# Kernel optimization log

Hardware: AMD Instinct MI355X
Metric: run time of the kernel (lower is better)

The kernel has to match this reference:

```python
import jax, jax.numpy as jnp
import numpy as np

B, S, E, H = 2, 2048, 1024, 16
DK = E // H


def setup_inputs() -> dict:
    key = jax.random.key(0)
    ks = jax.random.split(key, 10)
    x = jax.random.normal(ks[0], (B, S, E), dtype=jnp.float32)
    mask = jax.random.randint(ks[1], (B, S, S), 0, 2).astype(bool)
    scale = 1.0 / np.sqrt(E)
    def lin(k):
        kw, kb = jax.random.split(k)
        W = jax.random.uniform(kw, (E, E), minval=-scale, maxval=scale, dtype=jnp.float32)
        b = jax.random.uniform(kb, (E,), minval=-scale, maxval=scale, dtype=jnp.float32)
        return W, b
    Wq, bq = lin(ks[2])
    Wk, bk = lin(ks[3])
    Wv, bv = lin(ks[4])
    Wo, bo = lin(ks[5])
    return {"x": x, "mask": mask, "Wq": Wq, "bq": bq, "Wk": Wk, "bk": bk,
            "Wv": Wv, "bv": bv, "Wo": Wo, "bo": bo}


def reference(x, mask, Wq, bq, Wk, bk, Wv, bv, Wo, bo):
    # projections (torch Linear: y = x @ W.T + b)
    q = x @ Wq.T + bq
    k = x @ Wk.T + bk
    v = x @ Wv.T + bv
    # separate heads: [B,S,E] -> [B,H,S,DK]
    def split(t):
        return t.reshape(B, S, H, DK).transpose(0, 2, 1, 3)
    q, k, v = split(q), split(k), split(v)
    scores = jnp.einsum("bhqd,bhkd->bhqk", q, k) / jnp.sqrt(jnp.float32(DK))
    # masked_fill: positions where mask is True get -1e9 (mask broadcast over heads)
    scores = jnp.where(mask[:, None, :, :], jnp.float32(-1e9), scores)
    attn = jax.nn.softmax(scores, axis=-1)  # dropout is identity in eval
    out = jnp.einsum("bhqk,bhkd->bhqd", attn, v)
    out = out.transpose(0, 2, 1, 3).reshape(B, S, E)  # combine heads
    return out @ Wo.T + bo
```

## Files before the change

kernel.cpp:

```cpp
#include <hip/hip_runtime.h>
#include <hip/hip_bf16.h>


typedef __attribute__((ext_vector_type(8))) short short8;
typedef __attribute__((ext_vector_type(4))) short s16x4;
typedef __attribute__((ext_vector_type(4))) float f32x4;
typedef __attribute__((ext_vector_type(2))) unsigned uint32x2;

#define MFMA16(a, b, c) __builtin_amdgcn_mfma_f32_16x16x32_bf16(a, b, c, 0, 0, 0)

#define BATCH 2
#define SEQ   2048
#define EMB   1024
#define HEADS 16
#define DKK   64
#define MROWS (BATCH * SEQ)

typedef __hip_bfloat16 bf16;
typedef unsigned long long u64;

static __device__ __forceinline__ short bf16b(float f) {
    union { bf16 h; short s; } u;
    u.h = __float2bfloat16(f);
    return u.s;
}
static __device__ __forceinline__ unsigned cvtpk(float lo, float hi) {
    unsigned r;
    asm("v_cvt_pk_bf16_f32 %0, %1, %2" : "=v"(r) : "v"(lo), "v"(hi));
    return r;
}
static __device__ __forceinline__ short8 ld8k(const bf16* p) {
    return *(const short8*)p;
}
static __device__ __forceinline__ short8 ld8kf(const float* p) {
    const f32x4 a = *(const f32x4*)p;
    const f32x4 b = *(const f32x4*)(p + 4);
    short8 r;
    r[0] = bf16b(a[0]); r[1] = bf16b(a[1]); r[2] = bf16b(a[2]); r[3] = bf16b(a[3]);
    r[4] = bf16b(b[0]); r[5] = bf16b(b[1]); r[6] = bf16b(b[2]); r[7] = bf16b(b[3]);
    return r;
}

static __device__ __forceinline__ void glds16(const bf16* g, bf16* l) {
    __builtin_amdgcn_global_load_lds(
        (const __attribute__((address_space(1))) void*)g,
        (__attribute__((address_space(3))) void*)l, 16, 0, 0);
}

__global__ void detect_kernel(const unsigned int* __restrict__ mw,
                              int* __restrict__ flags) {
    __shared__ int mbyte;
    if (threadIdx.x == 0) mbyte = 0;
    __syncthreads();
    int mb = 0;
    for (int i = threadIdx.x; i < 4096; i += 256)
        if (mw[i] > 1u) mb = 1;
    if (mb) atomicOr(&mbyte, 1);
    __syncthreads();
    if (threadIdx.x == 0) { flags[0] = 1; flags[1] = mbyte; }
}

__global__ __launch_bounds__(256) void pack_mask(
        const void* __restrict__ mp, unsigned* __restrict__ Mp,
        const int* __restrict__ flags) {
    const bool m8 = flags[1] != 0;
    const int T = blockIdx.x * 256 + threadIdx.x;
    const int lane = T & 63, rest = T >> 6;
    const int wvv = rest & 7;
    const int qb  = (rest >> 3) & 15;
    const int it  = (rest >> 7) & 31;
    const int b   = rest >> 12;
    const int l16 = lane & 15, quad = lane >> 4;
    const int q = qb * 128 + wvv * 16 + l16;
    const size_t rowb = ((size_t)(b * 2048 + q)) * 2048;
    const int k0 = it * 64 + quad * 4;

    unsigned out[4];
    if (m8) {
        const unsigned char* p8 = (const unsigned char*)mp;
#pragma unroll
        for (int j = 0; j < 4; ++j) {
            const unsigned v = *(const unsigned*)(p8 + rowb + k0 + j * 16);
            unsigned w = 0;
#pragma unroll
            for (int r = 0; r < 4; ++r)
                w |= ((((v >> (8 * r)) & 0xFFu) == 0u) ? 0xFFu : 0u) << (8 * r);
            out[j] = w;
        }
    } else {
        const int* p32 = (const int*)mp;
#pragma unroll
        for (int j = 0; j < 4; ++j) {
            const int4 v = *(const int4*)(p32 + rowb + k0 + j * 16);
            unsigned w = 0;
            w |=  (v.x == 0) ? 0xFFu : 0u;
            w |= ((v.y == 0) ? 0xFFu : 0u) << 8;
            w |= ((v.z == 0) ? 0xFFu : 0u) << 16;
            w |= ((v.w == 0) ? 0xFFu : 0u) << 24;
            out[j] = w;
        }
    }
    uint4* dst = (uint4*)(Mp + (size_t)rest * 256 + lane * 4);
    *dst = make_uint4(out[0], out[1], out[2], out[3]);
}

__global__ __launch_bounds__(256) void cvt_all(
        const float* __restrict__ x,  const float* __restrict__ wq,
        const float* __restrict__ wk, const float* __restrict__ wv,
        const float* __restrict__ wo,
        bf16* __restrict__ xb,  bf16* __restrict__ wqb,
        bf16* __restrict__ wkb, bf16* __restrict__ wvb,
        bf16* __restrict__ wob) {
    const int bid = blockIdx.x;
    const float* s; bf16* d; int base;
    if (bid < 2048)      { s = x;  d = xb;  base = bid; }
    else if (bid < 2560) { s = wq; d = wqb; base = bid - 2048; }
    else if (bid < 3072) { s = wk; d = wkb; base = bid - 2560; }
    else if (bid < 3584) { s = wv; d = wvb; base = bid - 3072; }
    else                 { s = wo; d = wob; base = bid - 3584; }
    const int i = (base * 256 + threadIdx.x) * 8;
    *(short8*)(d + i) = ld8kf(s + i);
}

__global__ __launch_bounds__(256) void gemm_qkv_staged(
        const bf16* __restrict__ X,
        const bf16* __restrict__ Wq, const bf16* __restrict__ Wk,
        const bf16* __restrict__ Wv,
        const float* __restrict__ bq, const float* __restrict__ bk,
        const float* __restrict__ bv,
        bf16* __restrict__ qo, bf16* __restrict__ ko, bf16* __restrict__ vo) {
    __shared__ bf16 As[2][128 * 32];
    __shared__ bf16 Bs[2][128 * 32];

    const int t = threadIdx.x, lane = t & 63;
    const int wv = t >> 6;
    const int mb = blockIdx.x / 24, nb = blockIdx.x % 24;
    const int m0 = mb * 128;
    const int n0g = nb * 128;
    const int sel = n0g >> 10;
    const int n0 = n0g & 1023;
    const bf16* W     = sel == 0 ? Wq : (sel == 1 ? Wk : Wv);
    const float* bias = sel == 0 ? bq : (sel == 1 ? bk : bv);
    bf16* out         = sel == 0 ? qo : (sel == 1 ? ko : vo);
    const float oscale = sel == 0 ? 0.18033688011f : 1.0f;

    const int wr = wv >> 1, wc = wv & 1;
    const int m_off = wr * 64, n_off = wc * 64;
    const int l16 = lane & 15, quad = lane >> 4;

    int srow[2], sg[2];
#pragma unroll
    for (int i = 0; i < 2; ++i) {
        const int c = i * 256 + t;
        srow[i] = c >> 2;
        sg[i]   = (c & 3) ^ (srow[i] & 3);
    }

    f32x4 acc[4][4];
#pragma unroll
    for (int i = 0; i < 4; ++i)
#pragma unroll
        for (int j = 0; j < 4; ++j)
            acc[i][j] = (f32x4){0.f, 0.f, 0.f, 0.f};

#pragma unroll
    for (int i = 0; i < 2; ++i) {
        glds16(X + (m0 + srow[i]) * 1024 + sg[i] * 8, &As[0][(i * 256 + t) * 8]);
        glds16(W + (n0 + srow[i]) * 1024 + sg[i] * 8, &Bs[0][(i * 256 + t) * 8]);
    }

    for (int it = 0; it < 32; ++it) {
        __syncthreads();
        if (it < 31) {
            const int ktn = (it + 1) * 32;
            const int nb_ = (it + 1) & 1;
#pragma unroll
            for (int i = 0; i < 2; ++i) {
                glds16(X + (m0 + srow[i]) * 1024 + ktn + sg[i] * 8,
                       &As[nb_][(i * 256 + t) * 8]);
                glds16(W + (n0 + srow[i]) * 1024 + ktn + sg[i] * 8,
                       &Bs[nb_][(i * 256 + t) * 8]);
            }
        }
        const bf16* Ab = As[it & 1];
        const bf16* Bb = Bs[it & 1];
        short8 af[4], bfr[4];
#pragma unroll
        for (int ii = 0; ii < 4; ++ii) {
            const int row = m_off + ii * 16 + l16;
            const int slot = quad ^ (row & 3);
            af[ii] = *(const short8*)(Ab + row * 32 + slot * 8);
        }
#pragma unroll
        for (int jj = 0; jj < 4; ++jj) {
            const int row = n_off + jj * 16 + l16;
            const int slot = quad ^ (row & 3);
            bfr[jj] = *(const short8*)(Bb + row * 32 + slot * 8);
        }
#pragma unroll
        for (int ii = 0; ii < 4; ++ii)
#pragma unroll
            for (int jj = 0; jj < 4; ++jj)
                acc[ii][jj] = MFMA16(af[ii], bfr[jj], acc[ii][jj]);
    }

#pragma unroll
    for (int j = 0; j < 4; ++j) {
        const int nl = n0 + n_off + j * 16 + l16;
        const float bj = bias[nl];
        const int h = nl >> 6, d = nl & 63;
#pragma unroll
        for (int i = 0; i < 4; ++i) {
#pragma unroll
            for (int r = 0; r < 4; ++r) {
                const int m = m0 + m_off + i * 16 + quad * 4 + r;
                const float v = (acc[i][j][r] + bj) * oscale;
                const int bb = m >> 11, ss = m & 2047;
                const int idx = (sel == 2)
                    ? ((bb * HEADS + h) * DKK + d) * SEQ + ss
                    : ((bb * HEADS + h) * SEQ + ss) * DKK + d;
                out[idx] = __float2bfloat16(v);
            }
        }
    }
}

__global__ __launch_bounds__(256) void gemm_out_staged(
        const bf16* __restrict__ X,
        const bf16* __restrict__ W, const float* __restrict__ bias,
        float* __restrict__ out) {
    __shared__ bf16 As[2][128 * 32];
    __shared__ bf16 Bs[2][64 * 32];

    const int t = threadIdx.x, lane = t & 63;
    const int wv = t >> 6;
    const int mb = blockIdx.x >> 4, nb = blockIdx.x & 15;
    const int m0 = mb * 128, n0 = nb * 64;
    const int wr = wv >> 1, wc = wv & 1;
    const int m_off = wr * 64, n_off = wc * 32;
    const int l16 = lane & 15, quad = lane >> 4;

    int srow[2], sg[2];
#pragma unroll
    for (int i = 0; i < 2; ++i) {
        const int c = i * 256 + t;
        srow[i] = c >> 2;
        sg[i]   = (c & 3) ^ (srow[i] & 3);
    }
    const int brow = t >> 2;
    const int bslot = (t & 3) ^ (brow & 3);

    f32x4 acc[4][2];
#pragma unroll
    for (int i = 0; i < 4; ++i)
#pragma unroll
        for (int j = 0; j < 2; ++j)
            acc[i][j] = (f32x4){0.f, 0.f, 0.f, 0.f};

#pragma unroll
    for (int i = 0; i < 2; ++i)
        glds16(X + (m0 + srow[i]) * 1024 + sg[i] * 8, &As[0][(i * 256 + t) * 8]);
    glds16(W + (n0 + brow) * 1024 + bslot * 8, &Bs[0][t * 8]);

    for (int it = 0; it < 32; ++it) {
        __syncthreads();
        if (it < 31) {
            const int ktn = (it + 1) * 32;
            const int nb_ = (it + 1) & 1;
#pragma unroll
            for (int i = 0; i < 2; ++i)
                glds16(X + (m0 + srow[i]) * 1024 + ktn + sg[i] * 8,
                       &As[nb_][(i * 256 + t) * 8]);
            glds16(W + (n0 + brow) * 1024 + ktn + bslot * 8, &Bs[nb_][t * 8]);
        }
        const bf16* Ab = As[it & 1];
        const bf16* Bb = Bs[it & 1];
        short8 af[4], bfr[2];
#pragma unroll
        for (int ii = 0; ii < 4; ++ii) {
            const int row = m_off + ii * 16 + l16;
            const int slot = quad ^ (row & 3);
            af[ii] = *(const short8*)(Ab + row * 32 + slot * 8);
        }
#pragma unroll
        for (int jj = 0; jj < 2; ++jj) {
            const int row = n_off + jj * 16 + l16;
            const int slot = quad ^ (row & 3);
            bfr[jj] = *(const short8*)(Bb + row * 32 + slot * 8);
        }
#pragma unroll
        for (int ii = 0; ii < 4; ++ii)
#pragma unroll
            for (int jj = 0; jj < 2; ++jj)
                acc[ii][jj] = MFMA16(af[ii], bfr[jj], acc[ii][jj]);
    }

#pragma unroll
    for (int j = 0; j < 2; ++j) {
        const int n = n0 + n_off + j * 16 + l16;
        const float bj = bias[n];
#pragma unroll
        for (int i = 0; i < 4; ++i) {
#pragma unroll
            for (int r = 0; r < 4; ++r) {
                const int m = m0 + m_off + i * 16 + quad * 4 + r;
                out[m * 1024 + n] = acc[i][j][r] + bj;
            }
        }
    }
}

__global__ __launch_bounds__(512, 4) void attn_kernel(
        const bf16* __restrict__ Qw,
        const bf16* __restrict__ Kw,
        const bf16* __restrict__ Vw,
        const unsigned* __restrict__ Mp,
        bf16* __restrict__ attn_out) {
    const int t = threadIdx.x;
    const int lane = t & 63;
    const int wv   = t >> 6;
    const int l16 = lane & 15, quad = lane >> 4;
    const int h = blockIdx.y, b = blockIdx.z;
    const int bh = b * HEADS + h;
    const int qb = blockIdx.x;
    const int qb0 = qb * 128;

    const bf16* Q  = Qw + bh * SEQ * DKK;
    const bf16* Kp = Kw + bh * SEQ * DKK;
    const bf16* Vt = Vw + bh * DKK * SEQ;

    __shared__ bf16 Ks[2][4096];
    __shared__ bf16 Vs[2][4096];
    __shared__ bf16 lds_p[8][16][72];

    short8 qf[2];
#pragma unroll
    for (int t2 = 0; t2 < 2; ++t2)
        qf[t2] = ld8k(Q + (qb0 + wv * 16 + l16) * DKK + t2 * 32 + quad * 8);

    const short ob = bf16b(1.0f);
    short8 ones;
#pragma unroll
    for (int e = 0; e < 8; ++e) ones[e] = ob;

    f32x4 o[4];
#pragma unroll
    for (int jd = 0; jd < 4; ++jd) o[jd] = (f32x4){0.f, 0.f, 0.f, 0.f};
    f32x4 lacc = (f32x4){0.f, 0.f, 0.f, 0.f};
    const f32x4 zacc = (f32x4){0.f, 0.f, 0.f, 0.f};

    const int srow = t >> 3;
    const int sg   = (t & 7) ^ (srow & 7);

    glds16(Kp + srow * DKK + sg * 8, &Ks[0][t * 8]);
    glds16(Vt + srow * SEQ + sg * 8, &Vs[0][t * 8]);

    const unsigned* mp_it = Mp + ((size_t)(b * 512 + qb) * 2048 + wv * 256 + lane * 4);

    for (int it = 0; it < SEQ / 64; ++it) {
        __syncthreads();
        if (it < SEQ / 64 - 1) {
            const int nb_ = (it + 1) & 1;
            const int ktn = (it + 1) * 64;
            glds16(Kp + (ktn + srow) * DKK + sg * 8, &Ks[nb_][t * 8]);
            glds16(Vt + srow * SEQ + ktn + sg * 8, &Vs[nb_][t * 8]);
        }

        const uint4 m4 = *(const uint4*)mp_it;
        mp_it += 32768;
        const unsigned m32[4] = {m4.x, m4.y, m4.z, m4.w};

        const bf16* Kb = Ks[it & 1];
        const bf16* Vb = Vs[it & 1];

        short8 kf[2][4];
#pragma unroll
        for (int t2 = 0; t2 < 2; ++t2)
#pragma unroll
            for (int j = 0; j < 4; ++j) {
                const int row = j * 16 + l16;
                const int slot = (t2 * 4 + quad) ^ (row & 7);
                kf[t2][j] = *(const short8*)(Kb + row * 64 + slot * 8);
            }

        f32x4 s[4];
        __builtin_amdgcn_s_setprio(1);
#pragma unroll
        for (int j = 0; j < 4; ++j) {
            s[j] = MFMA16(kf[0][j], qf[0], zacc);
            s[j] = MFMA16(kf[1][j], qf[1], s[j]);
        }
        __builtin_amdgcn_s_setprio(0);

#pragma unroll
        for (int j = 0; j < 4; ++j) {
            const float p0 = __builtin_exp2f(s[j][0]);
            const float p1 = __builtin_exp2f(s[j][1]);
            const float p2 = __builtin_exp2f(s[j][2]);
            const float p3 = __builtin_exp2f(s[j][3]);
            uint32x2 pw;
            pw[0] = cvtpk(p0, p1) & __builtin_amdgcn_perm(0u, m32[j], 0x01010000u);
            pw[1] = cvtpk(p2, p3) & __builtin_amdgcn_perm(0u, m32[j], 0x03030202u);
            *(uint32x2*)(&lds_p[wv][l16][j * 16 + quad * 4]) = pw;
        }

        __builtin_amdgcn_s_setprio(1);
#pragma unroll
        for (int t2 = 0; t2 < 2; ++t2) {
            short8 vf[4];
#pragma unroll
            for (int jd = 0; jd < 4; ++jd) {
                const int row = jd * 16 + l16;
                const int slot = (t2 * 4 + quad) ^ (row & 7);
                vf[jd] = *(const short8*)(Vb + row * 64 + slot * 8);
            }
            const short8 pf = *(const short8*)(&lds_p[wv][l16][t2 * 32 + quad * 8]);
            lacc = MFMA16(pf, ones, lacc);
#pragma unroll
            for (int jd = 0; jd < 4; ++jd)
                o[jd] = MFMA16(pf, vf[jd], o[jd]);
        }
        __builtin_amdgcn_s_setprio(0);
    }

#pragma unroll
    for (int r = 0; r < 4; ++r) {
        const float inv = 1.0f / lacc[r];
        const int q = qb0 + wv * 16 + quad * 4 + r;
#pragma unroll
        for (int jd = 0; jd < 4; ++jd)
            attn_out[(b * SEQ + q) * EMB + h * DKK + jd * 16 + l16] =
                __float2bfloat16(o[jd][r] * inv);
    }
}

extern "C" void kernel_launch(void* const* d_in, const int* in_sizes, int n_in,
                              void* d_out, int out_size, void* d_ws, size_t ws_size,
                              hipStream_t stream) {
    char* ws = (char*)d_ws;
    const size_t MB = 1024 * 1024;
    int*      flags = (int*)ws;
    bf16*     wob   = (bf16*)(ws + 256);
    bf16*     wqb   = (bf16*)(ws + 256 + 2 * MB);
    bf16*     wkb   = (bf16*)(ws + 256 + 4 * MB);
    bf16*     wvb   = (bf16*)(ws + 256 + 6 * MB);
    unsigned* Mp    = (unsigned*)(ws + 256 + 2 * MB);
    bf16*     xb    = (bf16*)(ws + 256 + 10 * MB);
    bf16*     k_ws  = (bf16*)(ws + 256 + 18 * MB);
    bf16*     attn_ws = xb;

    bf16* q_ws = (bf16*)d_out;
    bf16* v_ws = (bf16*)d_out + 4194304;

    detect_kernel<<<1, 256, 0, stream>>>((const unsigned int*)d_in[1], flags);

    cvt_all<<<4096, 256, 0, stream>>>(
        (const float*)d_in[0], (const float*)d_in[2], (const float*)d_in[4],
        (const float*)d_in[6], (const float*)d_in[8],
        xb, wqb, wkb, wvb, wob);

    gemm_qkv_staged<<<768, 256, 0, stream>>>(
        xb, wqb, wkb, wvb,
        (const float*)d_in[3], (const float*)d_in[5], (const float*)d_in[7],
        q_ws, k_ws, v_ws);

    pack_mask<<<2048, 256, 0, stream>>>(d_in[1], Mp, flags);

    attn_kernel<<<dim3(SEQ / 128, HEADS, BATCH), 512, 0, stream>>>(
        q_ws, k_ws, v_ws, Mp, attn_ws);

    gemm_out_staged<<<512, 256, 0, stream>>>(
        attn_ws, wob, (const float*)d_in[9], (float*)d_out);
}
```

Measured before the change: 249.9 us.

## Switch attention to 32x32x16 MFMA with register-resident P via permlane32 swap

Rewrites the attention kernel so each wave handles 32 query rows using 32x32x16 bf16 MFMAs instead of 16x16x32. The P tile is kept in registers and rearranged into the B-operand layout with v_permlane32_swap, removing the per-wave LDS round-trip for probabilities. The block shrinks to 4 waves with each thread staging two K/V chunks, and the mask packing kernel is relaid out to match the new fragment layout. Occupancy hints and register pressure change, since the 16-element accumulators raise VGPR use.

```diff
diff --git a/kernel.cpp b/kernel.cpp
--- a/kernel.cpp
+++ b/kernel.cpp
@@ -3,21 +3,19 @@
 
 
 typedef __attribute__((ext_vector_type(8))) short short8;
-typedef __attribute__((ext_vector_type(4))) short s16x4;
 typedef __attribute__((ext_vector_type(4))) float f32x4;
-typedef __attribute__((ext_vector_type(2))) unsigned uint32x2;
+typedef __attribute__((ext_vector_type(16))) float f32x16;
 
 #define MFMA16(a, b, c) __builtin_amdgcn_mfma_f32_16x16x32_bf16(a, b, c, 0, 0, 0)
+#define MFMA32(a, b, c) __builtin_amdgcn_mfma_f32_32x32x16_bf16(a, b, c, 0, 0, 0)
 
 #define BATCH 2
 #define SEQ   2048
 #define EMB   1024
 #define HEADS 16
 #define DKK   64
-#define MROWS (BATCH * SEQ)
 
 typedef __hip_bfloat16 bf16;
-typedef unsigned long long u64;
 
 static __device__ __forceinline__ short bf16b(float f) {
     union { bf16 h; short s; } u;
@@ -28,6 +26,9 @@
     unsigned r;
     asm("v_cvt_pk_bf16_f32 %0, %1, %2" : "=v"(r) : "v"(lo), "v"(hi));
     return r;
+}
+static __device__ __forceinline__ void swap32(unsigned &a, unsigned &b) {
+    asm("v_permlane32_swap_b32 %0, %1" : "+v"(a), "+v"(b));
 }
 static __device__ __forceinline__ short8 ld8k(const bf16* p) {
     return *(const short8*)p;
@@ -65,43 +66,47 @@
         const int* __restrict__ flags) {
     const bool m8 = flags[1] != 0;
     const int T = blockIdx.x * 256 + threadIdx.x;
-    const int lane = T & 63, rest = T >> 6;
-    const int wvv = rest & 7;
-    const int qb  = (rest >> 3) & 15;
-    const int it  = (rest >> 7) & 31;
-    const int b   = rest >> 12;
-    const int l16 = lane & 15, quad = lane >> 4;
-    const int q = qb * 128 + wvv * 16 + l16;
+    const int lane = T & 63, g = T >> 6;
+    const int wvv = g & 3;
+    const int qb  = (g >> 2) & 15;
+    const int it  = (g >> 6) & 31;
+    const int b   = g >> 11;
+    const int l32 = lane & 31, hi = lane >> 5;
+    const int q = qb * 128 + wvv * 32 + l32;
     const size_t rowb = ((size_t)(b * 2048 + q)) * 2048;
-    const int k0 = it * 64 + quad * 4;
-
-    unsigned out[4];
+
+    unsigned out[8];
     if (m8) {
         const unsigned char* p8 = (const unsigned char*)mp;
 #pragma unroll
-        for (int j = 0; j < 4; ++j) {
-            const unsigned v = *(const unsigned*)(p8 + rowb + k0 + j * 16);
+        for (int k = 0; k < 8; ++k) {
+            const int kb = k >> 2, tt = (k >> 1) & 1, u = k & 1;
+            const int key0 = it * 64 + kb * 32 + tt * 16 + hi * 8 + u * 4;
+            const unsigned v = *(const unsigned*)(p8 + rowb + key0);
             unsigned w = 0;
 #pragma unroll
             for (int r = 0; r < 4; ++r)
                 w |= ((((v >> (8 * r)) & 0xFFu) == 0u) ? 0xFFu : 0u) << (8 * r);
-            out[j] = w;
+            out[k] = w;
         }
     } else {
         const int* p32 = (const int*)mp;
 #pragma unroll
-        for (int j = 0; j < 4; ++j) {
-            const int4 v = *(const int4*)(p32 + rowb + k0 + j * 16);
+        for (int k = 0; k < 8; ++k) {
+            const int kb = k >> 2, tt = (k >> 1) & 1, u = k & 1;
+            const int key0 = it * 64 + kb * 32 + tt * 16 + hi * 8 + u * 4;
+            const int4 v = *(const int4*)(p32 + rowb + key0);
             unsigned w = 0;
             w |=  (v.x == 0) ? 0xFFu : 0u;
             w |= ((v.y == 0) ? 0xFFu : 0u) << 8;
             w |= ((v.z == 0) ? 0xFFu : 0u) << 16;
             w |= ((v.w == 0) ? 0xFFu : 0u) << 24;
-            out[j] = w;
-        }
-    }
-    uint4* dst = (uint4*)(Mp + (size_t)rest * 256 + lane * 4);
-    *dst = make_uint4(out[0], out[1], out[2], out[3]);
+            out[k] = w;
+        }
+    }
+    unsigned* dst = Mp + (size_t)g * 512 + lane * 8;
+    *(uint4*)dst       = make_uint4(out[0], out[1], out[2], out[3]);
+    *(uint4*)(dst + 4) = make_uint4(out[4], out[5], out[6], out[7]);
 }
 
 __global__ __launch_bounds__(256) void cvt_all(
@@ -310,7 +315,7 @@
     }
 }
 
-__global__ __launch_bounds__(512, 4) void attn_kernel(
+__global__ __launch_bounds__(256, 2) void attn_kernel(
         const bf16* __restrict__ Qw,
         const bf16* __restrict__ Kw,
         const bf16* __restrict__ Vw,
@@ -319,7 +324,7 @@
     const int t = threadIdx.x;
     const int lane = t & 63;
     const int wv   = t >> 6;
-    const int l16 = lane & 15, quad = lane >> 4;
+    const int l32 = lane & 31, hi = lane >> 5;
     const int h = blockIdx.y, b = blockIdx.z;
     const int bh = b * HEADS + h;
     const int qb = blockIdx.x;
@@ -331,106 +336,158 @@
 
     __shared__ bf16 Ks[2][4096];
     __shared__ bf16 Vs[2][4096];
-    __shared__ bf16 lds_p[8][16][72];
-
-    short8 qf[2];
-#pragma unroll
-    for (int t2 = 0; t2 < 2; ++t2)
-        qf[t2] = ld8k(Q + (qb0 + wv * 16 + l16) * DKK + t2 * 32 + quad * 8);
+
+    short8 qf[4];
+#pragma unroll
+    for (int ks = 0; ks < 4; ++ks)
+        qf[ks] = ld8k(Q + (qb0 + wv * 32 + l32) * DKK + ks * 16 + hi * 8);
 
     const short ob = bf16b(1.0f);
     short8 ones;
 #pragma unroll
     for (int e = 0; e < 8; ++e) ones[e] = ob;
 
-    f32x4 o[4];
-#pragma unroll
-    for (int jd = 0; jd < 4; ++jd) o[jd] = (f32x4){0.f, 0.f, 0.f, 0.f};
-    f32x4 lacc = (f32x4){0.f, 0.f, 0.f, 0.f};
-    const f32x4 zacc = (f32x4){0.f, 0.f, 0.f, 0.f};
-
-    const int srow = t >> 3;
-    const int sg   = (t & 7) ^ (srow & 7);
-
-    glds16(Kp + srow * DKK + sg * 8, &Ks[0][t * 8]);
-    glds16(Vt + srow * SEQ + sg * 8, &Vs[0][t * 8]);
-
-    const unsigned* mp_it = Mp + ((size_t)(b * 512 + qb) * 2048 + wv * 256 + lane * 4);
-
-    for (int it = 0; it < SEQ / 64; ++it) {
+    f32x16 oA = {}, oB = {}, lacc = {};
+    const f32x16 z16 = {};
+
+    int srow[2], sg[2];
+#pragma unroll
+    for (int i = 0; i < 2; ++i) {
+        const int c = i * 256 + t;
+        srow[i] = c >> 3;
+        sg[i]   = (c & 7) ^ (srow[i] & 7);
+    }
+#pragma unroll
+    for (int i = 0; i < 2; ++i)
+        glds16(Kp + srow[i] * DKK + sg[i] * 8, &Ks[0][(i * 256 + t) * 8]);
+#pragma unroll
+    for (int i = 0; i < 2; ++i)
+        glds16(Vt + srow[i] * SEQ + sg[i] * 8, &Vs[0][(i * 256 + t) * 8]);
+
+    const unsigned* mp_it =
+        Mp + ((size_t)((b * 32) * 16 + qb) * 4 + wv) * 512 + lane * 8;
+
+    for (int it = 0; it < 32; ++it) {
         __syncthreads();
-        if (it < SEQ / 64 - 1) {
+        if (it < 31) {
             const int nb_ = (it + 1) & 1;
             const int ktn = (it + 1) * 64;
-            glds16(Kp + (ktn + srow) * DKK + sg * 8, &Ks[nb_][t * 8]);
-            glds16(Vt + srow * SEQ + ktn + sg * 8, &Vs[nb_][t * 8]);
-        }
-
-        const uint4 m4 = *(const uint4*)mp_it;
+#pragma unroll
+            for (int i = 0; i < 2; ++i)
+                glds16(Kp + (ktn + srow[i]) * DKK + sg[i] * 8,
+                       &Ks[nb_][(i * 256 + t) * 8]);
+#pragma unroll
+            for (int i = 0; i < 2; ++i)
+                glds16(Vt + srow[i] * SEQ + ktn + sg[i] * 8,
+                       &Vs[nb_][(i * 256 + t) * 8]);
+        }
+        const uint4 mA = *(const uint4*)mp_it;
+        const uint4 mB = *(const uint4*)(mp_it + 4);
         mp_it += 32768;
-        const unsigned m32[4] = {m4.x, m4.y, m4.z, m4.w};
 
         const bf16* Kb = Ks[it & 1];
         const bf16* Vb = Vs[it & 1];
 
-        short8 kf[2][4];
-#pragma unroll
-        for (int t2 = 0; t2 < 2; ++t2)
-#pragma unroll
-            for (int j = 0; j < 4; ++j) {
-                const int row = j * 16 + l16;
-                const int slot = (t2 * 4 + quad) ^ (row & 7);
-                kf[t2][j] = *(const short8*)(Kb + row * 64 + slot * 8);
-            }
-
-        f32x4 s[4];
+        short8 kf0[4], kf1[4];
+#pragma unroll
+        for (int ks = 0; ks < 4; ++ks) {
+            const int sl = (((ks * 2 + hi) ^ (l32 & 7))) * 8;
+            kf0[ks] = *(const short8*)(Kb + l32 * 64 + sl);
+            kf1[ks] = *(const short8*)(Kb + (32 + l32) * 64 + sl);
+        }
+
+        f32x16 s0, s1;
         __builtin_amdgcn_s_setprio(1);
-#pragma unroll
-        for (int j = 0; j < 4; ++j) {
-            s[j] = MFMA16(kf[0][j], qf[0], zacc);
-            s[j] = MFMA16(kf[1][j], qf[1], s[j]);
-        }
+        s0 = MFMA32(kf0[0], qf[0], z16);
+        s0 = MFMA32(kf0[1], qf[1], s0);
+        s0 = MFMA32(kf0[2], qf[2], s0);
+        s0 = MFMA32(kf0[3], qf[3], s0);
+        s1 = MFMA32(kf1[0], qf[0], z16);
+        s1 = MFMA32(kf1[1], qf[1], s1);
+        s1 = MFMA32(kf1[2], qf[2], s1);
+        s1 = MFMA32(kf1[3], qf[3], s1);
         __builtin_amdgcn_s_setprio(0);
 
-#pragma unroll
-        for (int j = 0; j < 4; ++j) {
-            const float p0 = __builtin_exp2f(s[j][0]);
-            const float p1 = __builtin_exp2f(s[j][1]);
-            const float p2 = __builtin_exp2f(s[j][2]);
-            const float p3 = __builtin_exp2f(s[j][3]);
-            uint32x2 pw;
-            pw[0] = cvtpk(p0, p1) & __builtin_amdgcn_perm(0u, m32[j], 0x01010000u);
-            pw[1] = cvtpk(p2, p3) & __builtin_amdgcn_perm(0u, m32[j], 0x03030202u);
-            *(uint32x2*)(&lds_p[wv][l16][j * 16 + quad * 4]) = pw;
-        }
-
-        __builtin_amdgcn_s_setprio(1);
-#pragma unroll
-        for (int t2 = 0; t2 < 2; ++t2) {
-            short8 vf[4];
-#pragma unroll
-            for (int jd = 0; jd < 4; ++jd) {
-                const int row = jd * 16 + l16;
-                const int slot = (t2 * 4 + quad) ^ (row & 7);
-                vf[jd] = *(const short8*)(Vb + row * 64 + slot * 8);
-            }
-            const short8 pf = *(const short8*)(&lds_p[wv][l16][t2 * 32 + quad * 8]);
-            lacc = MFMA16(pf, ones, lacc);
-#pragma unroll
-            for (int jd = 0; jd < 4; ++jd)
-                o[jd] = MFMA16(pf, vf[jd], o[jd]);
-        }
-        __builtin_amdgcn_s_setprio(0);
-    }
-
-#pragma unroll
-    for (int r = 0; r < 4; ++r) {
+        {
+            unsigned c0 = cvtpk(__builtin_exp2f(s0[0]),  __builtin_exp2f(s0[1]));
+            unsigned c1 = cvtpk(__builtin_exp2f(s0[2]),  __builtin_exp2f(s0[3]));
+            unsigned c2 = cvtpk(__builtin_exp2f(s0[4]),  __builtin_exp2f(s0[5]));
+            unsigned c3 = cvtpk(__builtin_exp2f(s0[6]),  __builtin_exp2f(s0[7]));
+            unsigned c4 = cvtpk(__builtin_exp2f(s0[8]),  __builtin_exp2f(s0[9]));
+            unsigned c5 = cvtpk(__builtin_exp2f(s0[10]), __builtin_exp2f(s0[11]));
+            unsigned c6 = cvtpk(__builtin_exp2f(s0[12]), __builtin_exp2f(s0[13]));
+            unsigned c7 = cvtpk(__builtin_exp2f(s0[14]), __builtin_exp2f(s0[15]));
+            swap32(c0, c2); swap32(c1, c3); swap32(c4, c6); swap32(c5, c7);
+            union { short8 v; unsigned w[4]; } p0, p1;
+            p0.w[0] = c0 & __builtin_amdgcn_perm(0u, mA.x, 0x01010000u);
+            p0.w[1] = c1 & __builtin_amdgcn_perm(0u, mA.x, 0x03030202u);
+            p0.w[2] = c2 & __builtin_amdgcn_perm(0u, mA.y, 0x01010000u);
+            p0.w[3] = c3 & __builtin_amdgcn_perm(0u, mA.y, 0x03030202u);
+            p1.w[0] = c4 & __builtin_amdgcn_perm(0u, mA.z, 0x01010000u);
+            p1.w[1] = c5 & __builtin_amdgcn_perm(0u, mA.z, 0x03030202u);
+            p1.w[2] = c6 & __builtin_amdgcn_perm(0u, mA.w, 0x01010000u);
+            p1.w[3] = c7 & __builtin_amdgcn_perm(0u, mA.w, 0x03030202u);
+
+            const int sl0 = ((0 + hi) ^ (l32 & 7)) * 8;
+            const int sl1 = ((2 + hi) ^ (l32 & 7)) * 8;
+            const short8 vf00 = *(const short8*)(Vb + l32 * 64 + sl0);
+            const short8 vf10 = *(const short8*)(Vb + (32 + l32) * 64 + sl0);
+            const short8 vf01 = *(const short8*)(Vb + l32 * 64 + sl1);
+            const short8 vf11 = *(const short8*)(Vb + (32 + l32) * 64 + sl1);
+            __builtin_amdgcn_s_setprio(1);
+            lacc = MFMA32(p0.v, ones, lacc);
+            oA = MFMA32(p0.v, vf00, oA);
+            oB = MFMA32(p0.v, vf10, oB);
+            lacc = MFMA32(p1.v, ones, lacc);
+            oA = MFMA32(p1.v, vf01, oA);
+            oB = MFMA32(p1.v, vf11, oB);
+            __builtin_amdgcn_s_setprio(0);
+        }
+        {
+            unsigned c0 = cvtpk(__builtin_exp2f(s1[0]),  __builtin_exp2f(s1[1]));
+            unsigned c1 = cvtpk(__builtin_exp2f(s1[2]),  __builtin_exp2f(s1[3]));
+            unsigned c2 = cvtpk(__builtin_exp2f(s1[4]),  __builtin_exp2f(s1[5]));
+            unsigned c3 = cvtpk(__builtin_exp2f(s1[6]),  __builtin_exp2f(s1[7]));
+            unsigned c4 = cvtpk(__builtin_exp2f(s1[8]),  __builtin_exp2f(s1[9]));
+            unsigned c5 = cvtpk(__builtin_exp2f(s1[10]), __builtin_exp2f(s1[11]));
+            unsigned c6 = cvtpk(__builtin_exp2f(s1[12]), __builtin_exp2f(s1[13]));
+            unsigned c7 = cvtpk(__builtin_exp2f(s1[14]), __builtin_exp2f(s1[15]));
+            swap32(c0, c2); swap32(c1, c3); swap32(c4, c6); swap32(c5, c7);
+            union { short8 v; unsigned w[4]; } p0, p1;
+            p0.w[0] = c0 & __builtin_amdgcn_perm(0u, mB.x, 0x01010000u);
+            p0.w[1] = c1 & __builtin_amdgcn_perm(0u, mB.x, 0x03030202u);
+            p0.w[2] = c2 & __builtin_amdgcn_perm(0u, mB.y, 0x01010000u);
+            p0.w[3] = c3 & __builtin_amdgcn_perm(0u, mB.y, 0x03030202u);
+            p1.w[0] = c4 & __builtin_amdgcn_perm(0u, mB.z, 0x01010000u);
+            p1.w[1] = c5 & __builtin_amdgcn_perm(0u, mB.z, 0x03030202u);
+            p1.w[2] = c6 & __builtin_amdgcn_perm(0u, mB.w, 0x01010000u);
+            p1.w[3] = c7 & __builtin_amdgcn_perm(0u, mB.w, 0x03030202u);
+
+            const int sl0 = ((4 + hi) ^ (l32 & 7)) * 8;
+            const int sl1 = ((6 + hi) ^ (l32 & 7)) * 8;
+            const short8 vf00 = *(const short8*)(Vb + l32 * 64 + sl0);
+            const short8 vf10 = *(const short8*)(Vb + (32 + l32) * 64 + sl0);
+            const short8 vf01 = *(const short8*)(Vb + l32 * 64 + sl1);
+            const short8 vf11 = *(const short8*)(Vb + (32 + l32) * 64 + sl1);
+            __builtin_amdgcn_s_setprio(1);
+            lacc = MFMA32(p0.v, ones, lacc);
+            oA = MFMA32(p0.v, vf00, oA);
+            oB = MFMA32(p0.v, vf10, oB);
+            lacc = MFMA32(p1.v, ones, lacc);
+            oA = MFMA32(p1.v, vf01, oA);
+            oB = MFMA32(p1.v, vf11, oB);
+            __builtin_amdgcn_s_setprio(0);
+        }
+    }
+
+#pragma unroll
+    for (int r = 0; r < 16; ++r) {
+        const int qrow = (r & 3) + 8 * (r >> 2) + 4 * hi;
         const float inv = 1.0f / lacc[r];
-        const int q = qb0 + wv * 16 + quad * 4 + r;
-#pragma unroll
-        for (int jd = 0; jd < 4; ++jd)
-            attn_out[(b * SEQ + q) * EMB + h * DKK + jd * 16 + l16] =
-                __float2bfloat16(o[jd][r] * inv);
+        const int q = qb0 + wv * 32 + qrow;
+        bf16* orow = attn_out + (b * SEQ + q) * EMB + h * DKK;
+        orow[l32]      = __float2bfloat16(oA[r] * inv);
+        orow[32 + l32] = __float2bfloat16(oB[r] * inv);
     }
 }
 
@@ -464,9 +521,9 @@
         (const float*)d_in[3], (const float*)d_in[5], (const float*)d_in[7],
         q_ws, k_ws, v_ws);
 
-    pack_mask<<<2048, 256, 0, stream>>>(d_in[1], Mp, flags);
-
-    attn_kernel<<<dim3(SEQ / 128, HEADS, BATCH), 512, 0, stream>>>(
+    pack_mask<<<1024, 256, 0, stream>>>(d_in[1], Mp, flags);
+
+    attn_kernel<<<dim3(SEQ / 128, HEADS, BATCH), 256, 0, stream>>>(
         q_ws, k_ws, v_ws, Mp, attn_ws);
 
     gemm_out_staged<<<512, 256, 0, stream>>>(
```

Result: no change. 250.6 us (+0.3%).
